# Performance work log

Hardware: AMD Instinct MI355X
Metric: run time of the kernel (lower is better)

Reference implementation:

```python
import jax, jax.numpy as jnp
import numpy as np

K = 7          # kernel_size
PAD = K // 2
NAZ, NEL = 12, 5
HID = 64
IC = 2         # input_channels == num_instruments
OC = 2         # output_channels (stereo)
EPS = 1e-5


def conv1d_same(x, w, b):
    # x: (N, Cin, T), w: (Cout, Cin, K) -> (N, Cout, T); cross-correlation like torch
    y = jax.lax.conv_general_dilated(x, w, (1,), 'SAME',
                                     dimension_numbers=('NCH', 'OIH', 'NCH'))
    return y + b[None, :, None]


def batchnorm(x, g, bt):
    # training-mode BatchNorm1d: biased batch stats over (N, T)
    mean = x.mean(axis=(0, 2), keepdims=True)
    var = x.var(axis=(0, 2), keepdims=True)
    return (x - mean) * jax.lax.rsqrt(var + EPS) * g[None, :, None] + bt[None, :, None]


def lrelu(x):
    return jnp.where(x >= 0, x, 0.2 * x)


def setup_inputs() -> dict:
    key = jax.random.key(0)
    ks = jax.random.split(key, 16)
    d = {}
    d['x'] = jax.random.normal(ks[0], (8, IC, 131072), dtype=jnp.float32)
    # spatial_param_net
    d['W1'] = jax.random.normal(ks[1], (HID, IC, K), dtype=jnp.float32) * 0.1
    d['b1'] = jnp.zeros((HID,), jnp.float32)
    d['g1'] = jnp.ones((HID,), jnp.float32)
    d['be1'] = jnp.zeros((HID,), jnp.float32)
    d['W2'] = jax.random.normal(ks[2], (2 * HID, HID, K), dtype=jnp.float32) * 0.05
    d['b2'] = jnp.zeros((2 * HID,), jnp.float32)
    d['g2'] = jnp.ones((2 * HID,), jnp.float32)
    d['be2'] = jnp.zeros((2 * HID,), jnp.float32)
    d['W3'] = jax.random.normal(ks[3], (IC * 3, 2 * HID, K), dtype=jnp.float32) * 0.05
    d['b3'] = jnp.zeros((IC * 3,), jnp.float32)
    # HRTF table: (num_azimuth*num_elevation, output_channels, K)
    d['hrtf'] = jax.random.normal(ks[4], (NAZ * NEL, OC, K), dtype=jnp.float32)
    # binaural_renderer (first conv in-channels = input_channels = 2)
    d['RW1'] = jax.random.normal(ks[5], (HID, IC, K), dtype=jnp.float32) * 0.1
    d['rb1'] = jnp.zeros((HID,), jnp.float32)
    d['rg1'] = jnp.ones((HID,), jnp.float32)
    d['rbe1'] = jnp.zeros((HID,), jnp.float32)
    d['RW2'] = jax.random.normal(ks[6], (2 * HID, HID, K), dtype=jnp.float32) * 0.05
    d['rb2'] = jnp.zeros((2 * HID,), jnp.float32)
    d['rg2'] = jnp.ones((2 * HID,), jnp.float32)
    d['rbe2'] = jnp.zeros((2 * HID,), jnp.float32)
    d['RW3'] = jax.random.normal(ks[7], (OC, 2 * HID, K), dtype=jnp.float32) * 0.05
    d['rb3'] = jnp.zeros((OC,), jnp.float32)
    return d


def reference(x, W1, b1, g1, be1, W2, b2, g2, be2, W3, b3, hrtf,
              RW1, rb1, rg1, rbe1, RW2, rb2, rg2, rbe2, RW3, rb3):
    B, I, T = x.shape
    # spatial parameter network
    h = lrelu(batchnorm(conv1d_same(x, W1, b1), g1, be1))
    h = lrelu(batchnorm(conv1d_same(h, W2, b2), g2, be2))
    sp = jnp.tanh(conv1d_same(h, W3, b3)).reshape(B, I, 3, T)
    # only t=0 of azimuth/elevation/distance is used (matches torch loop)
    az = (sp[:, :, 0, 0] + 1.0) * 0.5 * (NAZ - 1)
    el = (sp[:, :, 1, 0] + 1.0) * 0.5 * (NEL - 1)
    dist = (sp[:, :, 2, 0] + 1.0) * 0.5 * 0.9 + 0.1      # (B, I)
    az_i = jnp.clip(az.astype(jnp.int32), 0, NAZ - 1)
    el_i = jnp.clip(el.astype(jnp.int32), 0, NEL - 1)
    idx = el_i * NAZ + az_i                               # (B, I)
    wg = hrtf[idx]                                        # (B, I, OC, K) gathered filters
    # per-(b,i) conv1d with its gathered HRTF filter, scale by distance, sum over instruments
    xp = jnp.pad(x, ((0, 0), (0, 0), (PAD, PAD)))
    windows = jnp.stack([xp[:, :, k:k + T] for k in range(K)], axis=2)  # (B, I, K, T)
    summed = jnp.einsum('bikt,bick,bi->bct', windows, wg, dist)          # (B, OC, T)
    # binaural renderer
    h = lrelu(batchnorm(conv1d_same(summed, RW1, rb1), rg1, rbe1))
    h = lrelu(batchnorm(conv1d_same(h, RW2, rb2), rg2, rbe2))
    return jnp.tanh(conv1d_same(h, RW3, rb3))
```

## Files before the change

kernel.cpp:

```cpp
#include <hip/hip_runtime.h>
#include <hip/hip_fp16.h>
#include <cstddef>


#define TLEN 131072
#define NB 8
#define NICH 2
#define NHID 64
#define NH2 128
#define EPSV 1e-5f
#define CNTF 1048576.0f
#define FT 120
#define FGRID 1093
#define XCH 2048

typedef _Float16 f16x8 __attribute__((ext_vector_type(8)));
typedef float f32x4 __attribute__((ext_vector_type(4)));

__device__ __forceinline__ float lrelu(float v) { return v >= 0.f ? v : 0.2f * v; }
__device__ __forceinline__ unsigned short h16(float v) {
  return __half_as_ushort(__float2half(v));
}
__device__ __forceinline__ float fh16(unsigned short u) {
  return __half2float(__ushort_as_half(u));
}

__global__ __launch_bounds__(256) void prep_weights(
    const float* __restrict__ W2c, const float* __restrict__ RW2c,
    const float* __restrict__ RW3c,
    const float* __restrict__ W1c, const float* __restrict__ RW1c,
    unsigned short* __restrict__ w2sp, unsigned short* __restrict__ w2re,
    unsigned short* __restrict__ w3g,
    unsigned short* __restrict__ w1sp, unsigned short* __restrict__ w1re)
{
  int e = blockIdx.x * 256 + threadIdx.x;
  if (e < 114688) {
    int e2 = (e >= 57344) ? e - 57344 : e;
    int frag = e2 >> 9, within = e2 & 511;
    int c = frag >> 3, mt = frag & 7;
    int mn = within >> 5, kk = within & 31;
    int o = mt * 16 + mn;
    int tap = c >> 1, ch = (c & 1) * 32 + kk;
    const float* src = (e >= 57344) ? RW2c : W2c;
    unsigned short* dst = (e >= 57344) ? w2re : w2sp;
    dst[e2] = h16(src[(o * 64 + ch) * 7 + tap]);
  } else if (e < 116736) {
    int e2 = e - 114688;
    int c = e2 >> 9, within = e2 & 511;
    int m = within >> 5, kk = within & 31;
    int ch = c * 32 + kk;
    w3g[e2] = (m < 14) ? h16(RW3c[((m / 7) * 128 + ch) * 7 + (m % 7)])
                       : (unsigned short)0;
  } else if (e < 120832) {
    int e2 = e - 116736;
    int which = (e2 >= 2048);
    int e3 = e2 & 2047;
    int m = e3 >> 9, w = e3 & 511;
    int mn = w >> 5, K = w & 31;
    int i = K >> 4, kk = K & 15;
    const float* src = which ? RW1c : W1c;
    unsigned short* dst = which ? w1re : w1sp;
    dst[e3] = (kk < 7) ? h16(src[(m * 16 + mn) * 14 + i * 7 + kk])
                       : (unsigned short)0;
  }
}

__global__ __launch_bounds__(256) void xcorr_stats(
    const float* __restrict__ z, float* __restrict__ partials)
{
  const int b = blockIdx.x >> 6;
  const int t0 = (blockIdx.x & 63) * XCH;
  __shared__ float zs[2][XCH + 8];
  __shared__ float redx[4][30];
  for (int i = 0; i < 2; ++i)
    for (int j = threadIdx.x; j < XCH + 7; j += 256) {
      int tg = t0 + j;
      zs[i][j] = (tg < TLEN) ? z[(b * 2 + i) * TLEN + tg] : 0.f;
    }
  __syncthreads();

  float acc[30];
  #pragma unroll
  for (int q = 0; q < 30; ++q) acc[q] = 0.f;
  const int tb = threadIdx.x * 8;
  #pragma unroll
  for (int tt = 0; tt < 8; ++tt) {
    int j = tb + tt;
    float z0 = zs[0][j], z1 = zs[1][j];
    acc[28] += z0; acc[29] += z1;
    #pragma unroll
    for (int d = 0; d < 7; ++d) {
      float a0 = zs[0][j + d], a1 = zs[1][j + d];
      acc[d]      += z0 * a0;
      acc[7 + d]  += z0 * a1;
      acc[14 + d] += z1 * a0;
      acc[21 + d] += z1 * a1;
    }
  }
  #pragma unroll
  for (int q = 0; q < 30; ++q)
    #pragma unroll
    for (int m = 1; m <= 32; m <<= 1)
      acc[q] += __shfl_xor(acc[q], m, 64);
  const int lane = threadIdx.x & 63, wv = threadIdx.x >> 6;
  if (lane == 0)
    #pragma unroll
    for (int q = 0; q < 30; ++q) redx[wv][q] = acc[q];
  __syncthreads();
  if (threadIdx.x < 30)
    partials[blockIdx.x * 30 + threadIdx.x] =
        redx[0][threadIdx.x] + redx[1][threadIdx.x] +
        redx[2][threadIdx.x] + redx[3][threadIdx.x];
}

__global__ __launch_bounds__(256) void assemble_coef1(
    const float* __restrict__ partials, int nblocks,
    const float* __restrict__ W1c, const float* __restrict__ b1c,
    const float* __restrict__ g, const float* __restrict__ be,
    float* __restrict__ coef)
{
  __shared__ float R[30];
  __shared__ float pr[8][30];
  __shared__ float w1s[64 * 14];
  for (int e = threadIdx.x; e < 64 * 14; e += 256) w1s[e] = W1c[e];
  if (threadIdx.x < 240) {
    int q = threadIdx.x % 30, chunk = threadIdx.x / 30;
    float s = 0.f;
    for (int j = chunk; j < nblocks; j += 8) s += partials[j * 30 + q];
    pr[chunk][q] = s;
  }
  __syncthreads();
  if (threadIdx.x < 30) {
    float s = 0.f;
    #pragma unroll
    for (int c = 0; c < 8; ++c) s += pr[c][threadIdx.x];
    R[threadIdx.x] = s;
  }
  __syncthreads();
  if (threadIdx.x < 64) {
    int o = threadIdx.x;
    const float* w = &w1s[o * 14];
    float b1v = b1c[o];
    float sy = 0.f;
    #pragma unroll
    for (int i = 0; i < 2; ++i)
      #pragma unroll
      for (int k = 0; k < 7; ++k) sy += w[i * 7 + k] * R[28 + i];
    float syy = 0.f;
    #pragma unroll
    for (int i = 0; i < 2; ++i)
      #pragma unroll
      for (int k = 0; k < 7; ++k) {
        float wv = w[i * 7 + k];
        #pragma unroll
        for (int i2 = 0; i2 < 2; ++i2)
          #pragma unroll
          for (int k2 = 0; k2 < 7; ++k2) {
            int d = k2 - k;
            float r = (d >= 0) ? R[i * 14 + i2 * 7 + d]
                               : R[i2 * 14 + i * 7 - d];
            syy += wv * w[i2 * 7 + k2] * r;
          }
      }
    float S1 = CNTF * b1v + sy;
    float S2 = 2.f * b1v * S1 - CNTF * b1v * b1v + syy;
    float mean = S1 / CNTF;
    float var = S2 / CNTF - mean * mean;
    float a = g[o] * rsqrtf(var + EPSV);
    coef[o] = a;
    coef[64 + o] = be[o] - mean * a;
  }
}

__global__ __launch_bounds__(256) void reduce_coef(
    const float* __restrict__ partials, int nblocks, int C,
    const float* __restrict__ g, const float* __restrict__ be,
    float* __restrict__ coef)
{
  const int c = blockIdx.x;
  float s = 0.f, ss = 0.f;
  for (int j = threadIdx.x; j < nblocks; j += 256) {
    s  += partials[j * 2 * C + c];
    ss += partials[j * 2 * C + C + c];
  }
  #pragma unroll
  for (int off = 32; off >= 1; off >>= 1) {
    s  += __shfl_down(s, off, 64);
    ss += __shfl_down(ss, off, 64);
  }
  __shared__ float rs[4], rss[4];
  const int lane = threadIdx.x & 63, wv = threadIdx.x >> 6;
  if (lane == 0) { rs[wv] = s; rss[wv] = ss; }
  __syncthreads();
  if (threadIdx.x == 0) {
    float st  = rs[0] + rs[1] + rs[2] + rs[3];
    float sst = rss[0] + rss[1] + rss[2] + rss[3];
    float mean = st / CNTF;
    float var  = sst / CNTF - mean * mean;
    float a = g[c] * rsqrtf(var + EPSV);
    coef[c] = a;
    coef[C + c] = be[c] - mean * a;
  }
}

__device__ __forceinline__ void stage_x(
    int t0, int xoff, const float* __restrict__ xin, int b, float* xs)
{
  for (int e = threadIdx.x; e < 2 * 168; e += 256) {
    int i = e / 168, j = e % 168;
    int tg = t0 - xoff + j;
    xs[e] = (tg >= 0 && tg < TLEN) ? xin[(b * NICH + i) * TLEN + tg] : 0.f;
  }
}

template<int HOF>
__device__ __forceinline__ void h1_mfma(
    int t0, const float* xs, unsigned short* xw,
    const unsigned short* __restrict__ w1f,
    const float* __restrict__ coef1, const float* __restrict__ b1c,
    unsigned short* h1f)
{
  for (int e = threadIdx.x; e < 144 * 2; e += 256) {
    int n = e >> 1, i = e & 1;
    const float* xp = &xs[i * 168 + n];
    unsigned short hv[7];
    #pragma unroll
    for (int kk = 0; kk < 7; ++kk) hv[kk] = h16(xp[kk]);
    *(uint4*)(xw + n * 32 + i * 16) = make_uint4(
        hv[0] | ((unsigned)hv[1] << 16), hv[2] | ((unsigned)hv[3] << 16),
        hv[4] | ((unsigned)hv[5] << 16), (unsigned)hv[6]);
    *(uint4*)(xw + n * 32 + i * 16 + 8) = make_uint4(0, 0, 0, 0);
  }
  __syncthreads();

  const int lane = threadIdx.x & 63;
  const int wv = threadIdx.x >> 6;
  const int mn = lane & 15, quad = lane >> 4;
  f16x8 A1 = *(const f16x8*)(w1f + wv * 512 + mn * 32 + quad * 8);
  f32x4 acc1[9];
  #pragma unroll
  for (int nt = 0; nt < 9; ++nt) {
    f32x4 z = {0.f, 0.f, 0.f, 0.f};
    acc1[nt] = z;
  }
  #pragma unroll
  for (int nt = 0; nt < 9; ++nt) {
    f16x8 bb = *(const f16x8*)(xw + (nt * 16 + mn) * 32 + quad * 8);
    acc1[nt] = __builtin_amdgcn_mfma_f32_16x16x32_f16(A1, bb, acc1[nt], 0, 0, 0);
  }
  const int ch0 = wv * 16 + quad * 4;
  float a1v[4], dd[4];
  #pragma unroll
  for (int r = 0; r < 4; ++r) {
    a1v[r] = coef1[ch0 + r];
    dd[r]  = coef1[64 + ch0 + r] + a1v[r] * b1c[ch0 + r];
  }
  #pragma unroll
  for (int nt = 0; nt < 9; ++nt) {
    int n = nt * 16 + mn;
    int t = t0 - HOF + n;
    bool ok = (t >= 0) && (t < TLEN);
    unsigned us[4];
    #pragma unroll
    for (int r = 0; r < 4; ++r) {
      float v = lrelu(a1v[r] * acc1[nt][r] + dd[r]);
      us[r] = h16(ok ? v : 0.f);
    }
    *(uint2*)(h1f + n * 72 + ch0) =
        make_uint2(us[0] | (us[1] << 16), us[2] | (us[3] << 16));
  }
}

__global__ __launch_bounds__(256, 4) void conv2_stats_mfma(
    const float* __restrict__ xin,
    const unsigned short* __restrict__ w1f, const float* __restrict__ b1c,
    const float* __restrict__ coef1,
    const unsigned short* __restrict__ w2f,
    const float* __restrict__ b2c,
    float* __restrict__ partials)
{
  const int b  = blockIdx.x >> 10;
  const int t0 = (blockIdx.x & 1023) * 128;

  __shared__ __align__(16) char smem[31296];
  unsigned short* h1f = (unsigned short*)smem;
  float* xs = (float*)(smem + 20736);
  unsigned short* xw = (unsigned short*)(smem + 22080);
  float* redS = (float*)smem;
  float* redSS= (float*)(smem + 8704);

  stage_x(t0, 6, xin, b, xs);
  __syncthreads();
  h1_mfma<3>(t0, xs, xw, w1f, coef1, b1c, h1f);
  __syncthreads();

  const int lane = threadIdx.x & 63;
  const int wv = threadIdx.x >> 6;
  const int mn = lane & 15, quad = lane >> 4;

  f32x4 acc[2][8];
  #pragma unroll
  for (int mt = 0; mt < 2; ++mt)
    #pragma unroll
    for (int nt = 0; nt < 8; ++nt) {
      f32x4 z = {0.f, 0.f, 0.f, 0.f};
      acc[mt][nt] = z;
    }

  f16x8 ca[2], na[2];
  auto loadA = [&](int c, f16x8 (&A)[2]) {
    #pragma unroll
    for (int mt = 0; mt < 2; ++mt)
      A[mt] = *(const f16x8*)(w2f + (c * 8 + wv * 2 + mt) * 512 + mn * 32 + quad * 8);
  };
  loadA(0, ca);
  #pragma unroll
  for (int c = 0; c < 14; ++c) {
    if (c < 13) loadA(c + 1, na);
    const int tap = c >> 1;
    const int ch0 = (c & 1) * 32 + quad * 8;
    #pragma unroll
    for (int nt = 0; nt < 8; ++nt) {
      f16x8 bb = *(const f16x8*)(h1f + (nt * 16 + mn + tap) * 72 + ch0);
      acc[0][nt] = __builtin_amdgcn_mfma_f32_16x16x32_f16(ca[0], bb, acc[0][nt], 0, 0, 0);
      acc[1][nt] = __builtin_amdgcn_mfma_f32_16x16x32_f16(ca[1], bb, acc[1][nt], 0, 0, 0);
    }
    ca[0] = na[0]; ca[1] = na[1];
  }
  __syncthreads();

  #pragma unroll
  for (int mt = 0; mt < 2; ++mt)
    #pragma unroll
    for (int r = 0; r < 4; ++r) {
      int o = (wv * 2 + mt) * 16 + quad * 4 + r;
      float bo = b2c[o];
      float s = 0.f, ss = 0.f;
      #pragma unroll
      for (int nt = 0; nt < 8; ++nt) {
        float v = acc[mt][nt][r] + bo;
        s += v; ss += v * v;
      }
      redS[o * 17 + mn] = s;
      redSS[o * 17 + mn] = ss;
    }
  __syncthreads();
  {
    int o = threadIdx.x & 127;
    const float* src = (threadIdx.x < 128) ? redS : redSS;
    float s = 0.f;
    #pragma unroll
    for (int j = 0; j < 16; ++j) s += src[o * 17 + j];
    partials[blockIdx.x * 256 + threadIdx.x] = s;
  }
}

__global__ __launch_bounds__(256) void finalize_spatial(
    const float* __restrict__ x,
    const float* __restrict__ W1c, const float* __restrict__ b1c,
    const float* __restrict__ coef1,
    const float* __restrict__ W2c, const float* __restrict__ b2c,
    const float* __restrict__ coef2,
    const float* __restrict__ W3c, const float* __restrict__ b3c,
    const float* __restrict__ hrtf, float* __restrict__ wgbuf)
{
  __shared__ float xl[NB * 2 * 16];
  __shared__ float h1l[NB * 64 * 10];
  __shared__ float h2l[NB * NH2 * 4];
  __shared__ float sp[48];
  const int tid = threadIdx.x;
  {
    int bb = tid >> 5, i = (tid >> 4) & 1, j = tid & 15;
    int t = j - 6;
    xl[tid] = (t >= 0) ? x[(bb * 2 + i) * TLEN + t] : 0.f;
  }
  __syncthreads();
  for (int e = tid; e < NB * 64; e += 256) {
    int bb = e >> 6, ch = e & 63;
    float a1 = coef1[ch], d1 = coef1[64 + ch], bo = b1c[ch];
    for (int tt = 0; tt < 10; ++tt) {
      float acc = bo;
      #pragma unroll
      for (int i2 = 0; i2 < 2; ++i2)
        #pragma unroll
        for (int k = 0; k < 7; ++k)
          acc += xl[(bb * 2 + i2) * 16 + tt + k] * W1c[ch * 14 + i2 * 7 + k];
      float v = lrelu(a1 * acc + d1);
      h1l[(bb * 64 + ch) * 10 + tt] = (tt >= 3) ? v : 0.f;
    }
  }
  __syncthreads();
  for (int e = tid; e < NB * NH2; e += 256) {
    int bb = e >> 7, o = e & 127;
    float a2 = coef2[o], d2 = coef2[NH2 + o], bo = b2c[o];
    float acc[4] = {bo, bo, bo, bo};
    for (int i = 0; i < 64; ++i)
      #pragma unroll
      for (int k = 0; k < 7; ++k) {
        float w = W2c[(o * 64 + i) * 7 + k];
        #pragma unroll
        for (int t = 0; t < 4; ++t)
          acc[t] += h1l[(bb * 64 + i) * 10 + t + k] * w;
      }
    #pragma unroll
    for (int t = 0; t < 4; ++t)
      h2l[(bb * NH2 + o) * 4 + t] = lrelu(a2 * acc[t] + d2);
  }
  __syncthreads();
  if (tid < 48) {
    int bb = tid / 6, c3 = tid % 6;
    float acc = b3c[c3];
    for (int c = 0; c < NH2; ++c)
      #pragma unroll
      for (int k = 3; k < 7; ++k)
        acc += h2l[(bb * NH2 + c) * 4 + (k - 3)] * W3c[(c3 * NH2 + c) * 7 + k];
    sp[tid] = tanhf(acc);
  }
  __syncthreads();
  if (tid < 16) {
    int bb = tid >> 1, i = tid & 1;
    float az = (sp[bb * 6 + i * 3 + 0] + 1.f) * 0.5f * 11.f;
    float el = (sp[bb * 6 + i * 3 + 1] + 1.f) * 0.5f * 4.f;
    float dist = (sp[bb * 6 + i * 3 + 2] + 1.f) * 0.5f * 0.9f + 0.1f;
    int azi = min(max((int)az, 0), 11);
    int eli = min(max((int)el, 0), 4);
    int idx = eli * 12 + azi;
    for (int e = 0; e < 14; ++e)
      wgbuf[(bb * 2 + i) * 14 + e] = hrtf[idx * 14 + e] * dist;
  }
}

__global__ __launch_bounds__(256) void mix_kernel(
    const float* __restrict__ x, const float* __restrict__ wgbuf,
    float* __restrict__ summed)
{
  const int b = blockIdx.x >> 7;
  const int t0 = (blockIdx.x & 127) * 1024 + threadIdx.x * 4;
  float wv[2][2][7];
  #pragma unroll
  for (int i = 0; i < 2; ++i)
    #pragma unroll
    for (int c = 0; c < 2; ++c)
      #pragma unroll
      for (int k = 0; k < 7; ++k)
        wv[i][c][k] = wgbuf[(b * 2 + i) * 14 + c * 7 + k];
  float acc[2][4] = {{0.f, 0.f, 0.f, 0.f}, {0.f, 0.f, 0.f, 0.f}};
  #pragma unroll
  for (int i = 0; i < 2; ++i) {
    float xl[12];
    #pragma unroll
    for (int j = 0; j < 12; ++j) {
      int tg = t0 - 4 + j;
      xl[j] = (tg >= 0 && tg < TLEN) ? x[(b * 2 + i) * TLEN + tg] : 0.f;
    }
    #pragma unroll
    for (int c = 0; c < 2; ++c)
      #pragma unroll
      for (int k = 0; k < 7; ++k)
        #pragma unroll
        for (int tt = 0; tt < 4; ++tt)
          acc[c][tt] += xl[tt + k + 1] * wv[i][c][k];
  }
  #pragma unroll
  for (int c = 0; c < 2; ++c)
    *reinterpret_cast<float4*>(&summed[(b * 2 + c) * TLEN + t0]) =
        make_float4(acc[c][0], acc[c][1], acc[c][2], acc[c][3]);
}

__global__ __launch_bounds__(256, 4) void conv2_final_mfma(
    const float* __restrict__ xin,
    const unsigned short* __restrict__ w1f, const float* __restrict__ b1c,
    const float* __restrict__ coef1,
    const unsigned short* __restrict__ w2f,
    const float* __restrict__ b2c, const float* __restrict__ coef2,
    const unsigned short* __restrict__ w3g, const float* __restrict__ rb3c,
    float* __restrict__ out)
{
  const int b  = blockIdx.y;
  const int t0 = blockIdx.x * FT;

  __shared__ __align__(16) char smem[39936];
  unsigned short* h1f = (unsigned short*)smem;
  float* xs = (float*)(smem + 20736);
  unsigned short* xw = (unsigned short*)(smem + 22080);
  unsigned short* h2t = (unsigned short*)smem;
  unsigned short* dq  = (unsigned short*)(smem + 34816);

  stage_x(t0, 9, xin, b, xs);
  __syncthreads();
  h1_mfma<6>(t0, xs, xw, w1f, coef1, b1c, h1f);
  __syncthreads();

  const int lane = threadIdx.x & 63;
  const int wv = threadIdx.x >> 6;
  const int mn = lane & 15, quad = lane >> 4;

  f32x4 acc[2][8];
  #pragma unroll
  for (int mt = 0; mt < 2; ++mt)
    #pragma unroll
    for (int nt = 0; nt < 8; ++nt) {
      f32x4 z = {0.f, 0.f, 0.f, 0.f};
      acc[mt][nt] = z;
    }

  f16x8 ca[2], na[2];
  auto loadA = [&](int c, f16x8 (&A)[2]) {
    #pragma unroll
    for (int mt = 0; mt < 2; ++mt)
      A[mt] = *(const f16x8*)(w2f + (c * 8 + wv * 2 + mt) * 512 + mn * 32 + quad * 8);
  };
  loadA(0, ca);
  #pragma unroll
  for (int c = 0; c < 14; ++c) {
    if (c < 13) loadA(c + 1, na);
    const int tap = c >> 1;
    const int ch0 = (c & 1) * 32 + quad * 8;
    #pragma unroll
    for (int nt = 0; nt < 8; ++nt) {
      f16x8 bb = *(const f16x8*)(h1f + (nt * 16 + mn + tap) * 72 + ch0);
      acc[0][nt] = __builtin_amdgcn_mfma_f32_16x16x32_f16(ca[0], bb, acc[0][nt], 0, 0, 0);
      acc[1][nt] = __builtin_amdgcn_mfma_f32_16x16x32_f16(ca[1], bb, acc[1][nt], 0, 0, 0);
    }
    ca[0] = na[0]; ca[1] = na[1];
  }
  __syncthreads();

  #pragma unroll
  for (int nt = 0; nt < 8; ++nt) {
    int jp = nt * 16 + mn;
    int t = t0 - 3 + jp;
    bool ok = (t >= 0) && (t < TLEN);
    #pragma unroll
    for (int mt = 0; mt < 2; ++mt) {
      int obase = (wv * 2 + mt) * 16 + quad * 4;
      unsigned us[4];
      #pragma unroll
      for (int r = 0; r < 4; ++r) {
        int o = obase + r;
        float v = acc[mt][nt][r] + b2c[o];
        v = lrelu(coef2[o] * v + coef2[NH2 + o]);
        us[r] = h16(ok ? v : 0.f);
      }
      *(uint2*)(h2t + jp * 136 + obase) =
          make_uint2(us[0] | (us[1] << 16), us[2] | (us[3] << 16));
    }
  }
  __syncthreads();

  const int nt0 = wv * 2;
  f32x4 acc3[2];
  #pragma unroll
  for (int i = 0; i < 2; ++i) {
    f32x4 z = {0.f, 0.f, 0.f, 0.f};
    acc3[i] = z;
  }
  #pragma unroll
  for (int c = 0; c < 4; ++c) {
    f16x8 A3 = *(const f16x8*)(w3g + c * 512 + mn * 32 + quad * 8);
    #pragma unroll
    for (int i = 0; i < 2; ++i) {
      f16x8 bb = *(const f16x8*)(h2t + ((nt0 + i) * 16 + mn) * 136 + c * 32 + quad * 8);
      acc3[i] = __builtin_amdgcn_mfma_f32_16x16x32_f16(A3, bb, acc3[i], 0, 0, 0);
    }
  }
  #pragma unroll
  for (int i = 0; i < 2; ++i) {
    int n = (nt0 + i) * 16 + mn;
    unsigned us[4];
    #pragma unroll
    for (int r = 0; r < 4; ++r) us[r] = h16(acc3[i][r]);
    *(uint2*)(dq + n * 20 + quad * 4) =
        make_uint2(us[0] | (us[1] << 16), us[2] | (us[3] << 16));
  }
  __syncthreads();

  {
    int tid = threadIdx.x;
    if (tid < 240) {
      int oc = (tid >= FT) ? 1 : 0;
      int u = tid - oc * FT;
      float s = rb3c[oc];
      #pragma unroll
      for (int tap = 0; tap < 7; ++tap)
        s += fh16(dq[(u + tap) * 20 + oc * 7 + tap]);
      int t = t0 + u;
      if (t < TLEN) out[(b * 2 + oc) * TLEN + t] = tanhf(s);
    }
  }
}

extern "C" void kernel_launch(void* const* d_in, const int* in_sizes, int n_in,
                              void* d_out, int out_size, void* d_ws, size_t ws_size,
                              hipStream_t stream)
{
  (void)in_sizes; (void)n_in; (void)out_size; (void)ws_size;
  const float* x    = (const float*)d_in[0];
  const float* W1   = (const float*)d_in[1];
  const float* b1   = (const float*)d_in[2];
  const float* g1   = (const float*)d_in[3];
  const float* be1  = (const float*)d_in[4];
  const float* W2   = (const float*)d_in[5];
  const float* b2   = (const float*)d_in[6];
  const float* g2   = (const float*)d_in[7];
  const float* be2  = (const float*)d_in[8];
  const float* W3   = (const float*)d_in[9];
  const float* b3   = (const float*)d_in[10];
  const float* hrtf = (const float*)d_in[11];
  const float* RW1  = (const float*)d_in[12];
  const float* rb1  = (const float*)d_in[13];
  const float* rg1  = (const float*)d_in[14];
  const float* rbe1 = (const float*)d_in[15];
  const float* RW2  = (const float*)d_in[16];
  const float* rb2  = (const float*)d_in[17];
  const float* rg2  = (const float*)d_in[18];
  const float* rbe2 = (const float*)d_in[19];
  const float* RW3  = (const float*)d_in[20];
  const float* rb3  = (const float*)d_in[21];
  float* out = (float*)d_out;

  float* partialsB = (float*)d_out;

  char* ws = (char*)d_ws;
  float* partialsA      = (float*)(ws + 0);
  float* summed         = (float*)(ws + 524288);
  float* coef1          = (float*)(ws + 8912896);
  float* coef2          = (float*)(ws + 8913408);
  float* coefR1         = (float*)(ws + 8914432);
  float* coefR2         = (float*)(ws + 8914944);
  float* wgbuf          = (float*)(ws + 8915968);
  unsigned short* w2sp  = (unsigned short*)(ws + 8916992);
  unsigned short* w2re  = (unsigned short*)(ws + 9031680);
  unsigned short* w3g   = (unsigned short*)(ws + 9146368);
  unsigned short* w1sp  = (unsigned short*)(ws + 9150464);
  unsigned short* w1re  = (unsigned short*)(ws + 9154560);

  prep_weights<<<472, 256, 0, stream>>>(W2, RW2, RW3, W1, RW1,
                                        w2sp, w2re, w3g, w1sp, w1re);
  xcorr_stats<<<512, 256, 0, stream>>>(x, partialsA);
  assemble_coef1<<<1, 256, 0, stream>>>(partialsA, 512, W1, b1, g1, be1, coef1);
  conv2_stats_mfma<<<8192, 256, 0, stream>>>(x, w1sp, b1, coef1, w2sp, b2,
                                             partialsB);
  reduce_coef<<<128, 256, 0, stream>>>(partialsB, 8192, 128, g2, be2, coef2);
  finalize_spatial<<<1, 256, 0, stream>>>(x, W1, b1, coef1, W2, b2, coef2,
                                          W3, b3, hrtf, wgbuf);
  mix_kernel<<<1024, 256, 0, stream>>>(x, wgbuf, summed);
  xcorr_stats<<<512, 256, 0, stream>>>(summed, partialsA);
  assemble_coef1<<<1, 256, 0, stream>>>(partialsA, 512, RW1, rb1, rg1, rbe1, coefR1);
  conv2_stats_mfma<<<8192, 256, 0, stream>>>(summed, w1re, rb1, coefR1,
                                             w2re, rb2, partialsB);
  reduce_coef<<<128, 256, 0, stream>>>(partialsB, 8192, 128, rg2, rbe2, coefR2);
  conv2_final_mfma<<<dim3(FGRID, NB), 256, 0, stream>>>(
      summed, w1re, rb1, coefR1, w2re, rb2, coefR2, w3g, rb3, out);
}
```

Before: 665.8 us.

## Fuse mix with xcorr stats, retile final conv2 MFMA, use packed fp16 converts

Merges the HRTF mix kernel with the cross-correlation statistics pass, so the mixed signal is reduced from shared memory instead of being re-read from global memory by a separate launch. The final conv2 MFMA loop is retiled so each wave computes a 4x4 block of tiles instead of 2x8, which reuses each B fragment across four A fragments. Float-to-fp16 packing now uses the cvt_pkrtz intrinsic, which rounds toward zero instead of to nearest. The conv2 bias is folded into a precomputed BN shift in reduce_coef. The rounding change and the extra accumulators carry small precision and register-pressure risks.

New measurement: 732.6 us. +10.0%, slower.

```diff
diff --git a/kernel.cpp b/kernel.cpp
--- a/kernel.cpp
+++ b/kernel.cpp
@@ -23,6 +23,12 @@
 }
 __device__ __forceinline__ float fh16(unsigned short u) {
   return __half2float(__ushort_as_half(u));
+}
+__device__ __forceinline__ unsigned pk16(float a, float b) {
+  __fp16 p2[2];
+  *reinterpret_cast<__fp16 __attribute__((ext_vector_type(2)))*>(p2) =
+      __builtin_amdgcn_cvt_pkrtz(a, b);
+  return *reinterpret_cast<unsigned*>(p2);
 }
 
 __global__ __launch_bounds__(256) void prep_weights(
@@ -175,7 +181,7 @@
 __global__ __launch_bounds__(256) void reduce_coef(
     const float* __restrict__ partials, int nblocks, int C,
     const float* __restrict__ g, const float* __restrict__ be,
-    float* __restrict__ coef)
+    const float* __restrict__ b2, float* __restrict__ coef)
 {
   const int c = blockIdx.x;
   float s = 0.f, ss = 0.f;
@@ -198,8 +204,10 @@
     float mean = st / CNTF;
     float var  = sst / CNTF - mean * mean;
     float a = g[c] * rsqrtf(var + EPSV);
+    float d = be[c] - mean * a;
     coef[c] = a;
-    coef[C + c] = be[c] - mean * a;
+    coef[C + c] = d;
+    coef[2 * C + c] = a * b2[c] + d;
   }
 }
 
@@ -223,12 +231,9 @@
   for (int e = threadIdx.x; e < 144 * 2; e += 256) {
     int n = e >> 1, i = e & 1;
     const float* xp = &xs[i * 168 + n];
-    unsigned short hv[7];
-    #pragma unroll
-    for (int kk = 0; kk < 7; ++kk) hv[kk] = h16(xp[kk]);
     *(uint4*)(xw + n * 32 + i * 16) = make_uint4(
-        hv[0] | ((unsigned)hv[1] << 16), hv[2] | ((unsigned)hv[3] << 16),
-        hv[4] | ((unsigned)hv[5] << 16), (unsigned)hv[6]);
+        pk16(xp[0], xp[1]), pk16(xp[2], xp[3]),
+        pk16(xp[4], xp[5]), pk16(xp[6], 0.f));
     *(uint4*)(xw + n * 32 + i * 16 + 8) = make_uint4(0, 0, 0, 0);
   }
   __syncthreads();
@@ -260,14 +265,14 @@
     int n = nt * 16 + mn;
     int t = t0 - HOF + n;
     bool ok = (t >= 0) && (t < TLEN);
-    unsigned us[4];
+    float v[4];
     #pragma unroll
     for (int r = 0; r < 4; ++r) {
-      float v = lrelu(a1v[r] * acc1[nt][r] + dd[r]);
-      us[r] = h16(ok ? v : 0.f);
+      float u = lrelu(a1v[r] * acc1[nt][r] + dd[r]);
+      v[r] = ok ? u : 0.f;
     }
     *(uint2*)(h1f + n * 72 + ch0) =
-        make_uint2(us[0] | (us[1] << 16), us[2] | (us[3] << 16));
+        make_uint2(pk16(v[0], v[1]), pk16(v[2], v[3]));
   }
 }
 
@@ -430,27 +435,31 @@
   }
 }
 
-__global__ __launch_bounds__(256) void mix_kernel(
+__global__ __launch_bounds__(256) void mix_xcorr(
     const float* __restrict__ x, const float* __restrict__ wgbuf,
-    float* __restrict__ summed)
+    float* __restrict__ summed, float* __restrict__ partials)
 {
   const int b = blockIdx.x >> 7;
-  const int t0 = (blockIdx.x & 127) * 1024 + threadIdx.x * 4;
-  float wv[2][2][7];
+  const int t0 = (blockIdx.x & 127) * 1024;
+  __shared__ float smix[2][1032];
+  __shared__ float redx[4][30];
+  float wv2[2][2][7];
   #pragma unroll
   for (int i = 0; i < 2; ++i)
     #pragma unroll
     for (int c = 0; c < 2; ++c)
       #pragma unroll
       for (int k = 0; k < 7; ++k)
-        wv[i][c][k] = wgbuf[(b * 2 + i) * 14 + c * 7 + k];
+        wv2[i][c][k] = wgbuf[(b * 2 + i) * 14 + c * 7 + k];
+
+  const int tc = t0 + threadIdx.x * 4;
   float acc[2][4] = {{0.f, 0.f, 0.f, 0.f}, {0.f, 0.f, 0.f, 0.f}};
   #pragma unroll
   for (int i = 0; i < 2; ++i) {
     float xl[12];
     #pragma unroll
     for (int j = 0; j < 12; ++j) {
-      int tg = t0 - 4 + j;
+      int tg = tc - 4 + j;
       xl[j] = (tg >= 0 && tg < TLEN) ? x[(b * 2 + i) * TLEN + tg] : 0.f;
     }
     #pragma unroll
@@ -459,12 +468,65 @@
       for (int k = 0; k < 7; ++k)
         #pragma unroll
         for (int tt = 0; tt < 4; ++tt)
-          acc[c][tt] += xl[tt + k + 1] * wv[i][c][k];
-  }
-  #pragma unroll
-  for (int c = 0; c < 2; ++c)
-    *reinterpret_cast<float4*>(&summed[(b * 2 + c) * TLEN + t0]) =
+          acc[c][tt] += xl[tt + k + 1] * wv2[i][c][k];
+  }
+  #pragma unroll
+  for (int c = 0; c < 2; ++c) {
+    *reinterpret_cast<float4*>(&summed[(b * 2 + c) * TLEN + tc]) =
         make_float4(acc[c][0], acc[c][1], acc[c][2], acc[c][3]);
+    *reinterpret_cast<float4*>(&smix[c][threadIdx.x * 4]) =
+        make_float4(acc[c][0], acc[c][1], acc[c][2], acc[c][3]);
+  }
+  if (threadIdx.x < 7) {
+    int ct = t0 + 1024 + threadIdx.x;
+    #pragma unroll
+    for (int c = 0; c < 2; ++c) {
+      float s = 0.f;
+      #pragma unroll
+      for (int i = 0; i < 2; ++i)
+        #pragma unroll
+        for (int k = 0; k < 7; ++k) {
+          int tg = ct + k - 3;
+          float xv = (tg >= 0 && tg < TLEN) ? x[(b * 2 + i) * TLEN + tg] : 0.f;
+          s += xv * wv2[i][c][k];
+        }
+      smix[c][1024 + threadIdx.x] = (ct < TLEN) ? s : 0.f;
+    }
+  }
+  __syncthreads();
+
+  float a30[30];
+  #pragma unroll
+  for (int q = 0; q < 30; ++q) a30[q] = 0.f;
+  const int jb = threadIdx.x * 4;
+  #pragma unroll
+  for (int tt = 0; tt < 4; ++tt) {
+    int j = jb + tt;
+    float z0 = smix[0][j], z1 = smix[1][j];
+    a30[28] += z0; a30[29] += z1;
+    #pragma unroll
+    for (int d = 0; d < 7; ++d) {
+      float a0 = smix[0][j + d], a1 = smix[1][j + d];
+      a30[d]      += z0 * a0;
+      a30[7 + d]  += z0 * a1;
+      a30[14 + d] += z1 * a0;
+      a30[21 + d] += z1 * a1;
+    }
+  }
+  #pragma unroll
+  for (int q = 0; q < 30; ++q)
+    #pragma unroll
+    for (int m = 1; m <= 32; m <<= 1)
+      a30[q] += __shfl_xor(a30[q], m, 64);
+  const int lane = threadIdx.x & 63, wv = threadIdx.x >> 6;
+  if (lane == 0)
+    #pragma unroll
+    for (int q = 0; q < 30; ++q) redx[wv][q] = a30[q];
+  __syncthreads();
+  if (threadIdx.x < 30)
+    partials[blockIdx.x * 30 + threadIdx.x] =
+        redx[0][threadIdx.x] + redx[1][threadIdx.x] +
+        redx[2][threadIdx.x] + redx[3][threadIdx.x];
 }
 
 __global__ __launch_bounds__(256, 4) void conv2_final_mfma(
@@ -472,7 +534,7 @@
     const unsigned short* __restrict__ w1f, const float* __restrict__ b1c,
     const float* __restrict__ coef1,
     const unsigned short* __restrict__ w2f,
-    const float* __restrict__ b2c, const float* __restrict__ coef2,
+    const float* __restrict__ coef2,
     const unsigned short* __restrict__ w3g, const float* __restrict__ rb3c,
     float* __restrict__ out)
 {
@@ -494,21 +556,22 @@
   const int lane = threadIdx.x & 63;
   const int wv = threadIdx.x >> 6;
   const int mn = lane & 15, quad = lane >> 4;
-
-  f32x4 acc[2][8];
-  #pragma unroll
-  for (int mt = 0; mt < 2; ++mt)
-    #pragma unroll
-    for (int nt = 0; nt < 8; ++nt) {
+  const int mh = wv & 1, nh = wv >> 1;
+
+  f32x4 acc[4][4];
+  #pragma unroll
+  for (int m = 0; m < 4; ++m)
+    #pragma unroll
+    for (int i = 0; i < 4; ++i) {
       f32x4 z = {0.f, 0.f, 0.f, 0.f};
-      acc[mt][nt] = z;
-    }
-
-  f16x8 ca[2], na[2];
-  auto loadA = [&](int c, f16x8 (&A)[2]) {
-    #pragma unroll
-    for (int mt = 0; mt < 2; ++mt)
-      A[mt] = *(const f16x8*)(w2f + (c * 8 + wv * 2 + mt) * 512 + mn * 32 + quad * 8);
+      acc[m][i] = z;
+    }
+
+  f16x8 ca[4], na[4];
+  auto loadA = [&](int c, f16x8 (&A)[4]) {
+    #pragma unroll
+    for (int m = 0; m < 4; ++m)
+      A[m] = *(const f16x8*)(w2f + (c * 8 + mh * 4 + m) * 512 + mn * 32 + quad * 8);
   };
   loadA(0, ca);
   #pragma unroll
@@ -517,33 +580,34 @@
     const int tap = c >> 1;
     const int ch0 = (c & 1) * 32 + quad * 8;
     #pragma unroll
-    for (int nt = 0; nt < 8; ++nt) {
-      f16x8 bb = *(const f16x8*)(h1f + (nt * 16 + mn + tap) * 72 + ch0);
-      acc[0][nt] = __builtin_amdgcn_mfma_f32_16x16x32_f16(ca[0], bb, acc[0][nt], 0, 0, 0);
-      acc[1][nt] = __builtin_amdgcn_mfma_f32_16x16x32_f16(ca[1], bb, acc[1][nt], 0, 0, 0);
-    }
-    ca[0] = na[0]; ca[1] = na[1];
-  }
-  __syncthreads();
-
-  #pragma unroll
-  for (int nt = 0; nt < 8; ++nt) {
-    int jp = nt * 16 + mn;
+    for (int i = 0; i < 4; ++i) {
+      f16x8 bb = *(const f16x8*)(h1f + ((nh * 4 + i) * 16 + mn + tap) * 72 + ch0);
+      #pragma unroll
+      for (int m = 0; m < 4; ++m)
+        acc[m][i] = __builtin_amdgcn_mfma_f32_16x16x32_f16(ca[m], bb, acc[m][i], 0, 0, 0);
+    }
+    #pragma unroll
+    for (int m = 0; m < 4; ++m) ca[m] = na[m];
+  }
+  __syncthreads();
+
+  #pragma unroll
+  for (int i = 0; i < 4; ++i) {
+    int jp = (nh * 4 + i) * 16 + mn;
     int t = t0 - 3 + jp;
     bool ok = (t >= 0) && (t < TLEN);
     #pragma unroll
-    for (int mt = 0; mt < 2; ++mt) {
-      int obase = (wv * 2 + mt) * 16 + quad * 4;
-      unsigned us[4];
+    for (int m = 0; m < 4; ++m) {
+      int obase = (mh * 4 + m) * 16 + quad * 4;
+      float v[4];
       #pragma unroll
       for (int r = 0; r < 4; ++r) {
         int o = obase + r;
-        float v = acc[mt][nt][r] + b2c[o];
-        v = lrelu(coef2[o] * v + coef2[NH2 + o]);
-        us[r] = h16(ok ? v : 0.f);
+        float u = lrelu(coef2[o] * acc[m][i][r] + coef2[2 * NH2 + o]);
+        v[r] = ok ? u : 0.f;
       }
       *(uint2*)(h2t + jp * 136 + obase) =
-          make_uint2(us[0] | (us[1] << 16), us[2] | (us[3] << 16));
+          make_uint2(pk16(v[0], v[1]), pk16(v[2], v[3]));
     }
   }
   __syncthreads();
@@ -567,11 +631,8 @@
   #pragma unroll
   for (int i = 0; i < 2; ++i) {
     int n = (nt0 + i) * 16 + mn;
-    unsigned us[4];
-    #pragma unroll
-    for (int r = 0; r < 4; ++r) us[r] = h16(acc3[i][r]);
     *(uint2*)(dq + n * 20 + quad * 4) =
-        make_uint2(us[0] | (us[1] << 16), us[2] | (us[3] << 16));
+        make_uint2(pk16(acc3[i][0], acc3[i][1]), pk16(acc3[i][2], acc3[i][3]));
   }
   __syncthreads();
 
@@ -625,15 +686,15 @@
   float* partialsA      = (float*)(ws + 0);
   float* summed         = (float*)(ws + 524288);
   float* coef1          = (float*)(ws + 8912896);
-  float* coef2          = (float*)(ws + 8913408);
-  float* coefR1         = (float*)(ws + 8914432);
-  float* coefR2         = (float*)(ws + 8914944);
-  float* wgbuf          = (float*)(ws + 8915968);
-  unsigned short* w2sp  = (unsigned short*)(ws + 8916992);
-  unsigned short* w2re  = (unsigned short*)(ws + 9031680);
-  unsigned short* w3g   = (unsigned short*)(ws + 9146368);
-  unsigned short* w1sp  = (unsigned short*)(ws + 9150464);
-  unsigned short* w1re  = (unsigned short*)(ws + 9154560);
+  float* coef2          = (float*)(ws + 8914944);
+  float* coefR1         = (float*)(ws + 8916992);
+  float* coefR2         = (float*)(ws + 8919040);
+  float* wgbuf          = (float*)(ws + 8921088);
+  unsigned short* w2sp  = (unsigned short*)(ws + 8922112);
+  unsigned short* w2re  = (unsigned short*)(ws + 9036800);
+  unsigned short* w3g   = (unsigned short*)(ws + 9151488);
+  unsigned short* w1sp  = (unsigned short*)(ws + 9155584);
+  unsigned short* w1re  = (unsigned short*)(ws + 9159680);
 
   prep_weights<<<472, 256, 0, stream>>>(W2, RW2, RW3, W1, RW1,
                                         w2sp, w2re, w3g, w1sp, w1re);
@@ -641,15 +702,16 @@
   assemble_coef1<<<1, 256, 0, stream>>>(partialsA, 512, W1, b1, g1, be1, coef1);
   conv2_stats_mfma<<<8192, 256, 0, stream>>>(x, w1sp, b1, coef1, w2sp, b2,
                                              partialsB);
-  reduce_coef<<<128, 256, 0, stream>>>(partialsB, 8192, 128, g2, be2, coef2);
+  reduce_coef<<<128, 256, 0, stream>>>(partialsB, 8192, 128, g2, be2, b2, coef2);
   finalize_spatial<<<1, 256, 0, stream>>>(x, W1, b1, coef1, W2, b2, coef2,
                                           W3, b3, hrtf, wgbuf);
-  mix_kernel<<<1024, 256, 0, stream>>>(x, wgbuf, summed);
-  xcorr_stats<<<512, 256, 0, stream>>>(summed, partialsA);
-  assemble_coef1<<<1, 256, 0, stream>>>(partialsA, 512, RW1, rb1, rg1, rbe1, coefR1);
+  mix_xcorr<<<1024, 256, 0, stream>>>(x, wgbuf, summed, partialsA);
+  assemble_coef1<<<1, 256, 0, stream>>>(partialsA, 1024, RW1, rb1, rg1, rbe1,
+                                        coefR1);
   conv2_stats_mfma<<<8192, 256, 0, stream>>>(summed, w1re, rb1, coefR1,
                                              w2re, rb2, partialsB);
-  reduce_coef<<<128, 256, 0, stream>>>(partialsB, 8192, 128, rg2, rbe2, coefR2);
+  reduce_coef<<<128, 256, 0, stream>>>(partialsB, 8192, 128, rg2, rbe2, rb2,
+                                       coefR2);
   conv2_final_mfma<<<dim3(FGRID, NB), 256, 0, stream>>>(
-      summed, w1re, rb1, coefR1, w2re, rb2, coefR2, w3g, rb3, out);
-}
+      summed, w1re, rb1, coefR1, w2re, coefR2, w3g, rb3, out);
+}
```
